# Performance work log

Hardware: AMD Instinct MI355X
Metric: run time of the kernel (lower is better)

Reference implementation:

```python
import jax, jax.numpy as jnp
import numpy as np

N_NODES = 100000
DEG = 16          # regular-graph degree so degrees[start] > 0 for all nodes
STEPS = 32
D_FEAT = 16
MAXI32 = 2147483647


def setup_inputs() -> dict:
    key = jax.random.key(0)
    k1, k2, k3 = jax.random.split(key, 3)
    x = jax.random.normal(k1, (N_NODES, D_FEAT), dtype=jnp.float32)
    # CSR-style flat adjacency list: node v's neighbors are
    # adj_nodes[adj_offset[v] : adj_offset[v] + degrees[v]]
    adj_nodes = jax.random.randint(k2, (N_NODES * DEG,), 0, N_NODES, dtype=jnp.int32)
    adj_offset = (jnp.arange(N_NODES, dtype=jnp.int32) * DEG)
    degrees = jnp.full((N_NODES,), DEG, dtype=jnp.int32)
    # cache of random integers, one per (step, walk), as in the torch code
    choices = jax.random.randint(k3, (STEPS, N_NODES), 0, MAXI32, dtype=jnp.int32)
    return {"x": x, "adj_nodes": adj_nodes, "adj_offset": adj_offset,
            "degrees": degrees, "choices": choices}


def reference(x, adj_nodes, adj_offset, degrees, choices):
    """Non-backtracking random walk (Walker.sample_walks with start_p=1.0,
    all nodes having degree > 0, so start = arange(n)).
    Returns walks [steps+1, w] and walk_edges [steps, w]."""
    n = degrees.shape[0]
    nb_degrees = jnp.maximum(degrees - 1, 1)  # reduced degree for non-backtrack rewrite
    start = jnp.arange(n, dtype=jnp.int32)

    def step(carry, ch):
        prev, cur = carry                      # [w] previous / current nodes
        deg = degrees[cur]
        edge_idx = ch % deg                    # unweighted modulo edge choice
        chosen = adj_offset[cur] + edge_idx
        new = adj_nodes[chosen]
        bt = new == prev                       # backtracking walks
        # conditional rewrite: pick a different outgoing edge
        alt = adj_offset[cur] + (edge_idx + 1 + ch % nb_degrees[cur]) % deg
        chosen = jnp.where(bt, alt, chosen)
        new = jnp.where(bt, adj_nodes[alt], new)
        return (cur, new), (new, chosen)

    # prev = -1 at step 0 => bt is all-False, matching the i > 0 guard
    prev0 = jnp.full_like(start, -1)
    _, (nodes, walk_edges) = jax.lax.scan(step, (prev0, start), choices)
    walks = jnp.concatenate([start[None, :], nodes], axis=0)  # [steps+1, w]
    return walks, walk_edges
```

## Files before the change

### kernel.cpp

```cpp
#include <hip/hip_runtime.h>


#define DEG 16
#define CHAINS 2
#define NMAX 131072
#define PACK_BLOCK 256
#define ENT_MASK 0x3FFFFu

__device__ unsigned int g_pk32[(size_t)NMAX * 9 + 2];
__device__ int g_flag;

__global__ __launch_bounds__(PACK_BLOCK) void pack_check_kernel(
    const int* __restrict__ adj_nodes,
    const int* __restrict__ adj_offset,
    const int* __restrict__ degrees,
    int n, int epoch) {
    __shared__ __align__(16) unsigned int lds[PACK_BLOCK * 9];

    int tid = threadIdx.x;
    int blockStart = blockIdx.x * PACK_BLOCK;
    int v = blockStart + tid;

    bool bad = false;
    if (v < n) {
        bad = (degrees[v] != DEG) || (adj_offset[v] != v * DEG);

        const uint4* row4 = (const uint4*)(adj_nodes + (size_t)v * DEG);
        uint4 r[4];
        r[0] = row4[0]; r[1] = row4[1]; r[2] = row4[2]; r[3] = row4[3];
        const unsigned* rr = (const unsigned*)r;

        unsigned dw[9];
#pragma unroll
        for (int j = 0; j < 9; ++j) dw[j] = 0u;
#pragma unroll
        for (int e = 0; e < 16; ++e) {
            unsigned id = rr[e];
            if (id >= 262144u) bad = true;
            unsigned s   = 18u * (unsigned)e;
            unsigned d   = s >> 5;
            unsigned off = s & 31u;
            dw[d] |= id << off;
            if (off > 14u) dw[d + 1] |= id >> (32u - off);
        }
#pragma unroll
        for (int j = 0; j < 9; ++j) lds[tid * 9 + j] = dw[j];
    }
    __syncthreads();

    int rows = n - blockStart;
    if (rows > PACK_BLOCK) rows = PACK_BLOCK;
    unsigned int* dstBase = g_pk32 + (size_t)blockStart * 9;
    if (rows == PACK_BLOCK) {
        uint4* dst4 = (uint4*)dstBase;
        const uint4* src4 = (const uint4*)lds;
        for (int i = tid; i < (PACK_BLOCK * 9) / 4; i += PACK_BLOCK)
            dst4[i] = src4[i];
    } else {
        int ndw = rows * 9;
        for (int i = tid; i < ndw; i += PACK_BLOCK) dstBase[i] = lds[i];
    }

    if (bad) g_flag = epoch;
}

__global__ __launch_bounds__(256) void validate_kernel(
    const int* __restrict__ adj_nodes, int n, int epoch) {
    int v = blockIdx.x * blockDim.x + threadIdx.x;
    if (v >= n) return;
    const unsigned* row = g_pk32 + (size_t)v * 9;
    bool bad = false;
#pragma unroll
    for (int e = 0; e < 16; ++e) {
        unsigned s   = 18u * (unsigned)e;
        unsigned d   = s >> 5;
        unsigned off = s & 31u;
        uint2 q = *(const uint2*)(row + d);
        unsigned id = __builtin_amdgcn_alignbit(q.y, q.x, off) & ENT_MASK;
        if (id != (unsigned)adj_nodes[(size_t)v * DEG + e]) bad = true;
    }
    if (bad) g_flag = epoch;
}

template <int STEPS>
__global__ __launch_bounds__(64) void walker_fast4(
    const int* __restrict__ choices,
    int* __restrict__ out, int n, int h, int epoch,
    const int* __restrict__ adj_nodes,
    const int* __restrict__ adj_offset,
    const int* __restrict__ degrees) {

    int t = blockIdx.x * blockDim.x + threadIdx.x;
    if (t >= h) return;

    int* walks      = out;
    int* walk_edges = out + (STEPS + 1) * n;

    int w0 = t;
    int w1 = t + h;
    bool has1 = (w1 < n);
    int w1s = has1 ? w1 : w0;

    __builtin_nontemporal_store(w0, &walks[w0]);
    if (has1) __builtin_nontemporal_store(w1, &walks[w1]);

    if (g_flag != epoch) {
        int c0[STEPS], c1[STEPS];
#pragma unroll
        for (int i = 0; i < STEPS; ++i) {
            c0[i] = __builtin_nontemporal_load(&choices[i * n + w0]);
            c1[i] = __builtin_nontemporal_load(&choices[i * n + w1s]);
        }

        int prev0 = -1, cur0 = w0;
        int prev1 = -1, cur1 = w1s;
#pragma unroll
        for (int i = 0; i < STEPS; ++i) {
            unsigned ch0 = (unsigned)c0[i];
            unsigned ch1 = (unsigned)c1[i];
            unsigned e0 = ch0 & (DEG - 1);
            unsigned e1 = ch1 & (DEG - 1);

            const unsigned* row0 = g_pk32 + (size_t)(unsigned)cur0 * 9u;
            const unsigned* row1 = g_pk32 + (size_t)(unsigned)cur1 * 9u;

            unsigned s0 = 18u * e0, d0 = s0 >> 5, f0 = s0 & 31u;
            unsigned s1 = 18u * e1, d1 = s1 >> 5, f1 = s1 & 31u;

            uint2 q0 = *(const uint2*)(row0 + d0);
            uint2 q1 = *(const uint2*)(row1 + d1);

            int n00 = (int)(__builtin_amdgcn_alignbit(q0.y, q0.x, f0) & ENT_MASK);
            int n10 = (int)(__builtin_amdgcn_alignbit(q1.y, q1.x, f1) & ENT_MASK);

            int nw0 = n00, nw1 = n10;
            unsigned ef0 = e0, ef1 = e1;
            if (n00 == prev0) {
                unsigned a0 = (e0 + 1u + ch0 % (DEG - 1)) & (DEG - 1);
                unsigned sa = 18u * a0, da = sa >> 5, fa = sa & 31u;
                uint2 qa = *(const uint2*)(row0 + da);
                nw0 = (int)(__builtin_amdgcn_alignbit(qa.y, qa.x, fa) & ENT_MASK);
                ef0 = a0;
            }
            if (n10 == prev1) {
                unsigned a1 = (e1 + 1u + ch1 % (DEG - 1)) & (DEG - 1);
                unsigned sb = 18u * a1, db = sb >> 5, fb = sb & 31u;
                uint2 qb = *(const uint2*)(row1 + db);
                nw1 = (int)(__builtin_amdgcn_alignbit(qb.y, qb.x, fb) & ENT_MASK);
                ef1 = a1;
            }

            int ce0 = (cur0 << 4) + (int)ef0;
            int ce1 = (cur1 << 4) + (int)ef1;

            __builtin_nontemporal_store(nw0, &walks[(i + 1) * n + w0]);
            __builtin_nontemporal_store(ce0, &walk_edges[i * n + w0]);
            if (has1) {
                __builtin_nontemporal_store(nw1, &walks[(i + 1) * n + w1]);
                __builtin_nontemporal_store(ce1, &walk_edges[i * n + w1]);
            }
            prev0 = cur0; cur0 = nw0;
            prev1 = cur1; cur1 = nw1;
        }
    } else {
        for (int k = 0; k < 2; ++k) {
            int w = (k == 0) ? w0 : w1;
            if (w >= n) break;
            int prev = -1, cur = w;
            for (int i = 0; i < STEPS; ++i) {
                int chv = choices[i * n + w];
                int deg = degrees[cur];
                int off = adj_offset[cur];
                int nb  = deg - 1 > 1 ? deg - 1 : 1;

                int e      = chv % deg;
                int chosen = off + e;
                int alt    = off + (e + 1 + chv % nb) % deg;

                int nv0 = adj_nodes[chosen];
                int nv1 = adj_nodes[alt];

                bool bt = (nv0 == prev);
                int nw  = bt ? nv1 : nv0;
                walks[(i + 1) * n + w] = nw;
                walk_edges[i * n + w]  = bt ? alt : chosen;
                prev = cur;
                cur  = nw;
            }
        }
    }
}

__global__ __launch_bounds__(256) void walker_generic(
    const int* __restrict__ adj_nodes,
    const int* __restrict__ adj_offset,
    const int* __restrict__ degrees,
    const int* __restrict__ choices,
    int* __restrict__ out, int n, int steps) {

    int w = blockIdx.x * blockDim.x + threadIdx.x;
    if (w >= n) return;

    int* walks      = out;
    int* walk_edges = out + (steps + 1) * n;
    walks[w] = w;

    int prev = -1, cur = w;
    for (int i = 0; i < steps; ++i) {
        int chv = choices[i * n + w];
        int deg = degrees[cur];
        int off = adj_offset[cur];
        int nb  = deg - 1 > 1 ? deg - 1 : 1;

        int e      = chv % deg;
        int chosen = off + e;
        int alt    = off + (e + 1 + chv % nb) % deg;

        int nv0 = adj_nodes[chosen];
        int nv1 = adj_nodes[alt];

        bool bt = (nv0 == prev);
        int nw  = bt ? nv1 : nv0;
        walks[(i + 1) * n + w] = nw;
        walk_edges[i * n + w]  = bt ? alt : chosen;
        prev = cur;
        cur  = nw;
    }
}

extern "C" void kernel_launch(void* const* d_in, const int* in_sizes, int n_in,
                              void* d_out, int out_size, void* d_ws, size_t ws_size,
                              hipStream_t stream) {
    const int* adj_nodes  = (const int*)d_in[1];
    const int* adj_offset = (const int*)d_in[2];
    const int* degrees    = (const int*)d_in[3];
    const int* choices    = (const int*)d_in[4];
    int* out = (int*)d_out;

    int n     = in_sizes[2];
    int steps = in_sizes[4] / n;

    if (steps == 32 && n <= NMAX) {
        static int s_epoch = 0;
        int epoch = ++s_epoch;

        int pg = (n + PACK_BLOCK - 1) / PACK_BLOCK;
        pack_check_kernel<<<pg, PACK_BLOCK, 0, stream>>>(adj_nodes, adj_offset,
                                                         degrees, n, epoch);
        validate_kernel<<<pg, PACK_BLOCK, 0, stream>>>(adj_nodes, n, epoch);

        int h  = (n + CHAINS - 1) / CHAINS;
        int wb = 64, wg = (h + wb - 1) / wb;
        walker_fast4<32><<<wg, wb, 0, stream>>>(choices, out, n, h, epoch,
                                                adj_nodes, adj_offset, degrees);
    } else {
        int block = 256, grid = (n + block - 1) / block;
        walker_generic<<<grid, block, 0, stream>>>(adj_nodes, adj_offset,
                                                   degrees, choices, out, n, steps);
    }
}
```

Before: 104.9 us.

## Fold pack validation into pack kernel and speculatively load backtrack alternative

Moves the round-trip check of the packed 18-bit adjacency rows into the pack kernel, where it runs on registers, and drops the separate validate kernel launch along with its reread of global memory. The walker now always computes and loads the alternative edge alongside the primary one and selects with predicates instead of a divergent branch. This removes one launch and a pass over memory, and takes the backtrack load off the dependent chain. The cost is an extra gather per step per chain even when no backtrack occurs.

```diff
diff --git a/kernel.cpp b/kernel.cpp
--- a/kernel.cpp
+++ b/kernel.cpp
@@ -42,6 +42,15 @@
             unsigned off = s & 31u;
             dw[d] |= id << off;
             if (off > 14u) dw[d + 1] |= id >> (32u - off);
+        }
+#pragma unroll
+        for (int e = 0; e < 16; ++e) {
+            unsigned s   = 18u * (unsigned)e;
+            unsigned d   = s >> 5;
+            unsigned off = s & 31u;
+            unsigned hi  = (off > 14u) ? dw[d + 1] : 0u;
+            unsigned id  = __builtin_amdgcn_alignbit(hi, dw[d], off) & ENT_MASK;
+            if (id != rr[e]) bad = true;
         }
 #pragma unroll
         for (int j = 0; j < 9; ++j) lds[tid * 9 + j] = dw[j];
@@ -64,26 +73,8 @@
     if (bad) g_flag = epoch;
 }
 
-__global__ __launch_bounds__(256) void validate_kernel(
-    const int* __restrict__ adj_nodes, int n, int epoch) {
-    int v = blockIdx.x * blockDim.x + threadIdx.x;
-    if (v >= n) return;
-    const unsigned* row = g_pk32 + (size_t)v * 9;
-    bool bad = false;
-#pragma unroll
-    for (int e = 0; e < 16; ++e) {
-        unsigned s   = 18u * (unsigned)e;
-        unsigned d   = s >> 5;
-        unsigned off = s & 31u;
-        uint2 q = *(const uint2*)(row + d);
-        unsigned id = __builtin_amdgcn_alignbit(q.y, q.x, off) & ENT_MASK;
-        if (id != (unsigned)adj_nodes[(size_t)v * DEG + e]) bad = true;
-    }
-    if (bad) g_flag = epoch;
-}
-
 template <int STEPS>
-__global__ __launch_bounds__(64) void walker_fast4(
+__global__ __launch_bounds__(64) void walker_fast5(
     const int* __restrict__ choices,
     int* __restrict__ out, int n, int h, int epoch,
     const int* __restrict__ adj_nodes,
@@ -120,35 +111,33 @@
             unsigned ch1 = (unsigned)c1[i];
             unsigned e0 = ch0 & (DEG - 1);
             unsigned e1 = ch1 & (DEG - 1);
+            unsigned a0 = (e0 + 1u + ch0 % (DEG - 1)) & (DEG - 1);
+            unsigned a1 = (e1 + 1u + ch1 % (DEG - 1)) & (DEG - 1);
 
             const unsigned* row0 = g_pk32 + (size_t)(unsigned)cur0 * 9u;
             const unsigned* row1 = g_pk32 + (size_t)(unsigned)cur1 * 9u;
 
             unsigned s0 = 18u * e0, d0 = s0 >> 5, f0 = s0 & 31u;
             unsigned s1 = 18u * e1, d1 = s1 >> 5, f1 = s1 & 31u;
+            unsigned sa = 18u * a0, da = sa >> 5, fa = sa & 31u;
+            unsigned sb = 18u * a1, db = sb >> 5, fb = sb & 31u;
 
             uint2 q0 = *(const uint2*)(row0 + d0);
+            uint2 qa = *(const uint2*)(row0 + da);
             uint2 q1 = *(const uint2*)(row1 + d1);
+            uint2 qb = *(const uint2*)(row1 + db);
 
             int n00 = (int)(__builtin_amdgcn_alignbit(q0.y, q0.x, f0) & ENT_MASK);
+            int n0a = (int)(__builtin_amdgcn_alignbit(qa.y, qa.x, fa) & ENT_MASK);
             int n10 = (int)(__builtin_amdgcn_alignbit(q1.y, q1.x, f1) & ENT_MASK);
-
-            int nw0 = n00, nw1 = n10;
-            unsigned ef0 = e0, ef1 = e1;
-            if (n00 == prev0) {
-                unsigned a0 = (e0 + 1u + ch0 % (DEG - 1)) & (DEG - 1);
-                unsigned sa = 18u * a0, da = sa >> 5, fa = sa & 31u;
-                uint2 qa = *(const uint2*)(row0 + da);
-                nw0 = (int)(__builtin_amdgcn_alignbit(qa.y, qa.x, fa) & ENT_MASK);
-                ef0 = a0;
-            }
-            if (n10 == prev1) {
-                unsigned a1 = (e1 + 1u + ch1 % (DEG - 1)) & (DEG - 1);
-                unsigned sb = 18u * a1, db = sb >> 5, fb = sb & 31u;
-                uint2 qb = *(const uint2*)(row1 + db);
-                nw1 = (int)(__builtin_amdgcn_alignbit(qb.y, qb.x, fb) & ENT_MASK);
-                ef1 = a1;
-            }
+            int n1b = (int)(__builtin_amdgcn_alignbit(qb.y, qb.x, fb) & ENT_MASK);
+
+            bool bt0 = (n00 == prev0);
+            bool bt1 = (n10 == prev1);
+            int nw0 = bt0 ? n0a : n00;
+            int nw1 = bt1 ? n1b : n10;
+            unsigned ef0 = bt0 ? a0 : e0;
+            unsigned ef1 = bt1 ? a1 : e1;
 
             int ce0 = (cur0 << 4) + (int)ef0;
             int ce1 = (cur1 << 4) + (int)ef1;
@@ -247,11 +236,10 @@
         int pg = (n + PACK_BLOCK - 1) / PACK_BLOCK;
         pack_check_kernel<<<pg, PACK_BLOCK, 0, stream>>>(adj_nodes, adj_offset,
                                                          degrees, n, epoch);
-        validate_kernel<<<pg, PACK_BLOCK, 0, stream>>>(adj_nodes, n, epoch);
 
         int h  = (n + CHAINS - 1) / CHAINS;
         int wb = 64, wg = (h + wb - 1) / wb;
-        walker_fast4<32><<<wg, wb, 0, stream>>>(choices, out, n, h, epoch,
+        walker_fast5<32><<<wg, wb, 0, stream>>>(choices, out, n, h, epoch,
                                                 adj_nodes, adj_offset, degrees);
     } else {
         int block = 256, grid = (n + block - 1) / block;
```

New measurement: 105.4 us. About the same (+0.4%).
